# Performance work log

Measured on AMD Instinct MI355X. Metric: run time of the kernel, lower is better.

## Reference

```python
import jax, jax.numpy as jnp
import numpy as np

B_, L_, DM, DI, DS, DTR, DC = 1, 2048, 2048, 4096, 16, 128, 4


def setup_inputs() -> dict:
    key = jax.random.key(0)
    ks = jax.random.split(key, 8)
    s = lambda k, shape, scale: jax.random.normal(k, shape, jnp.float32) * scale
    inp = {
        "hidden_states": s(ks[0], (B_, L_, DM), 1.0),
        "in_proj_weight": s(ks[1], (2 * DI, DM), DM ** -0.5),
        "conv1d_weight": s(ks[2], (DI, 1, DC), DC ** -0.5),
        "x_proj_weight": s(ks[3], (DTR + 2 * DS, DI), DI ** -0.5),
        "dt_proj_weight": s(ks[4], (DI, DTR), DTR ** -0.5),
        "out_proj_weight": s(ks[5], (DM, DI), DI ** -0.5),
    }
    # dt_proj_bias = inverse-softplus of dt ~ LogUniform[1e-3, 0.1] (as in init_dtprojbias)
    dt = jnp.exp(jax.random.uniform(ks[6], (DI,), jnp.float32) * (np.log(0.1) - np.log(0.001)) + np.log(0.001))
    dt = jnp.clip(dt, 1e-4, None)
    inp["dt_proj_bias"] = dt + jnp.log(-jnp.expm1(-dt))
    # A_log init: log of repeat(arange(1, d_state+1)) per d_inner row
    inp["A_log"] = jnp.log(jnp.tile(jnp.arange(1, DS + 1, dtype=jnp.float32), (DI, 1)))
    inp["D"] = jnp.ones((DI,), jnp.float32)
    return inp


def reference(hidden_states, in_proj_weight, conv1d_weight, x_proj_weight,
              dt_proj_weight, dt_proj_bias, A_log, D, out_proj_weight):
    b, l, dm = hidden_states.shape
    di, ds = A_log.shape
    # in_proj: [b,l,dm] -> xz [b, 2*di, l]
    xz = jnp.einsum('ed,bld->bel', in_proj_weight, hidden_states)
    x, z = xz[:, :di], xz[:, di:]
    # depthwise causal conv1d (pad left d_conv-1, no bias) + SiLU
    x = jax.lax.conv_general_dilated(
        x, conv1d_weight, window_strides=(1,), padding=[(DC - 1, 0)],
        dimension_numbers=('NCH', 'OIH', 'NCH'), feature_group_count=di)
    x = jax.nn.silu(x)  # [b, di, l]
    # x_proj -> dt, B, C
    x_dbl = jnp.einsum('pd,bdl->blp', x_proj_weight, x)  # [b,l,dtr+2*ds]
    dt, Bc, Cc = jnp.split(x_dbl, [DTR, DTR + ds], axis=-1)
    delta = jnp.einsum('dr,blr->bld', dt_proj_weight, dt) + dt_proj_bias
    delta = jax.nn.softplus(delta)  # delta_softplus=True, delta_bias applied
    A = -jnp.exp(A_log)  # [di, ds]
    u = jnp.transpose(x, (0, 2, 1))  # [b,l,di]

    def step(h, inputs):
        d_t, B_t, C_t, u_t = inputs  # [b,di],[b,ds],[b,ds],[b,di]
        dA = jnp.exp(d_t[..., None] * A)                      # [b,di,ds]
        h = h * dA + (d_t * u_t)[..., None] * B_t[:, None, :]  # [b,di,ds]
        y = jnp.einsum('bdn,bn->bd', h, C_t)
        return h, y

    h0 = jnp.zeros((b, di, ds), hidden_states.dtype)
    xs = (jnp.swapaxes(delta, 0, 1), jnp.swapaxes(Bc, 0, 1),
          jnp.swapaxes(Cc, 0, 1), jnp.swapaxes(u, 0, 1))
    _, ys = jax.lax.scan(step, h0, xs)          # [l,b,di]
    y = jnp.swapaxes(ys, 0, 1) + u * D          # skip term u*D
    y = y * jax.nn.silu(jnp.transpose(z, (0, 2, 1)))  # gate
    return jnp.einsum('md,bld->blm', out_proj_weight, y)
```

## Files before the change

### kernel.cpp

```cpp
#include <hip/hip_runtime.h>
#include <hip/hip_bf16.h>

#define LSEQ 2048
#define DMODEL 2048
#define DINNER 4096
#define DSTATE 16
#define DTRANK 128
#define DCONV 4
#define DXP (DTRANK + 2*DSTATE)
#define NCHUNK 64
#define LCHUNK (LSEQ / NCHUNK)
#define KSPLIT 16

using bf16 = __hip_bfloat16;
typedef __attribute__((ext_vector_type(8))) short short8;
typedef __attribute__((ext_vector_type(4))) float float4v;

__device__ __forceinline__ float b2f(bf16 v) { return __bfloat162float(v); }
__device__ __forceinline__ bf16 f2b(float v) { return __float2bfloat16(v); }
__device__ __forceinline__ float bl16(unsigned u) { return __uint_as_float(u << 16); }
__device__ __forceinline__ float bh16(unsigned u) { return __uint_as_float(u & 0xffff0000u); }

__device__ __forceinline__ short f2bs(float v) {
    bf16 b = __float2bfloat16(v);
    union { bf16 b; short s; } u; u.b = b; return u.s;
}

__device__ __forceinline__ float fsilu(float x) {
    return x * __builtin_amdgcn_rcpf(1.0f + __expf(-x));
}

__device__ __forceinline__ short8 ld8(const float* p) {
    float4v f0 = *(const float4v*)p;
    float4v f1 = *(const float4v*)(p + 4);
    short8 r;
    r[0] = f2bs(f0[0]); r[1] = f2bs(f0[1]); r[2] = f2bs(f0[2]); r[3] = f2bs(f0[3]);
    r[4] = f2bs(f1[0]); r[5] = f2bs(f1[1]); r[6] = f2bs(f1[2]); r[7] = f2bs(f1[3]);
    return r;
}
__device__ __forceinline__ short8 ld8(const bf16* p) { return *(const short8*)p; }

template<typename CT> __device__ __forceinline__ CT cvtC(float v);
template<> __device__ __forceinline__ bf16  cvtC<bf16>(float v)  { return f2b(v); }
template<> __device__ __forceinline__ float cvtC<float>(float v) { return v; }

template<typename T> __device__ __forceinline__ float cvtL(T v);
template<> __device__ __forceinline__ float cvtL<bf16>(bf16 v)   { return b2f(v); }
template<> __device__ __forceinline__ float cvtL<float>(float v) { return v; }

__device__ __forceinline__ void glds16(const bf16* g, void* lds_base) {
    __builtin_amdgcn_global_load_lds(
        (const __attribute__((address_space(1))) void*)g,
        (__attribute__((address_space(3))) void*)lds_base, 16, 0, 0);
}

__global__ __launch_bounds__(256) void cvt4(
    const float* __restrict__ s0, bf16* __restrict__ d0, int n0,
    const float* __restrict__ s1, bf16* __restrict__ d1, int n1,
    const float* __restrict__ s2, bf16* __restrict__ d2, int n2,
    const float* __restrict__ s3, bf16* __restrict__ d3, int n3)
{
    const int b = blockIdx.x;
    const int nb0 = n0 >> 11, nb1 = n1 >> 11, nb2 = n2 >> 11;
    const float* s; bf16* d; int i;
    if (b < nb0)                  { s = s0; d = d0; i = b * 2048; }
    else if (b < nb0 + nb1)       { s = s1; d = d1; i = (b - nb0) * 2048; }
    else if (b < nb0 + nb1 + nb2) { s = s2; d = d2; i = (b - nb0 - nb1) * 2048; }
    else                          { s = s3; d = d3; i = (b - nb0 - nb1 - nb2) * 2048; }
    i += threadIdx.x * 8;
    *(short8*)(d + i) = ld8(s + i);
}

__global__ __launch_bounds__(256) void cvt1(
    const float* __restrict__ src, bf16* __restrict__ dst, int n)
{
    int i = (blockIdx.x * 256 + threadIdx.x) * 8;
    if (i >= n) return;
    *(short8*)(dst + i) = ld8(src + i);
}

#define GBAR  __builtin_amdgcn_s_barrier()
#define VMW4  asm volatile("s_waitcnt vmcnt(4)" ::: "memory")
#define VMW8  asm volatile("s_waitcnt vmcnt(8)" ::: "memory")
#define VMW0  asm volatile("s_waitcnt vmcnt(0)" ::: "memory")

#define LDA8(BASE, RB, AF) do {                                                \
  _Pragma("unroll") for (int mi_ = 0; mi_ < 4; ++mi_)                          \
  _Pragma("unroll") for (int kk_ = 0; kk_ < 2; ++kk_)                          \
    AF[mi_][kk_] = *(const short8*)((BASE) + (((RB) + mi_*16 + t16) << 6)      \
                                    + ((((kk_*4) + quad) ^ sw7) << 3));        \
} while (0)

#define LDB4(BASE, RB, BF) do {                                                \
  _Pragma("unroll") for (int nj_ = 0; nj_ < 2; ++nj_)                          \
  _Pragma("unroll") for (int kk_ = 0; kk_ < 2; ++kk_)                          \
    BF[nj_][kk_] = *(const short8*)((BASE) + (((RB) + nj_*16 + t16) << 6)      \
                                    + ((((kk_*4) + quad) ^ sw7) << 3));        \
} while (0)

#define MM16(AF, BF, MO, NO) do {                                              \
  _Pragma("unroll") for (int kk_ = 0; kk_ < 2; ++kk_)                          \
  _Pragma("unroll") for (int mi_ = 0; mi_ < 4; ++mi_)                          \
  _Pragma("unroll") for (int nj_ = 0; nj_ < 2; ++nj_)                          \
    acc[(MO)+mi_][(NO)+nj_] = __builtin_amdgcn_mfma_f32_16x16x32_bf16(         \
        AF[mi_][kk_], BF[nj_][kk_], acc[(MO)+mi_][(NO)+nj_], 0, 0, 0);         \
} while (0)

#define ST_ALO(tau) do { size_t ko_ = (size_t)(tau) << 6; int bo_ = ((tau)&1) << 15; \
  glds16(sA +       ko_, dA0 + bo_);                                           \
  glds16(sA + oA1 + ko_, dA1 + bo_); } while (0)
#define ST_AHI(tau) do { size_t ko_ = (size_t)(tau) << 6; int bo_ = ((tau)&1) << 15; \
  glds16(sA + oA2 + ko_, dA2 + bo_);                                           \
  glds16(sA + oA3 + ko_, dA3 + bo_); } while (0)
#define ST_BLO(tau) do { size_t ko_ = (size_t)(tau) << 6; int bo_ = ((tau)&1) << 15; \
  glds16(sB +       ko_, dB0 + bo_);                                           \
  glds16(sB + oB1 + ko_, dB1 + bo_); } while (0)
#define ST_BHI(tau) do { size_t ko_ = (size_t)(tau) << 6; int bo_ = ((tau)&1) << 15; \
  glds16(sB + oB2 + ko_, dB2 + bo_);                                           \
  glds16(sB + oB3 + ko_, dB3 + bo_); } while (0)

#define KSTEP(T, BI) do {                                                      \
    const bf16* Ab = As[BI];                                                   \
    const bf16* Bb = Bs[BI];                                                   \
    short8 af[4][2], b0[2][2], b1[2][2];                                       \
                                       \
    LDA8(Ab, wm, af);                                                          \
    LDB4(Bb, wn, b0);                                                          \
    if ((T) + 1 < NT) { ST_AHI((T) + 1); ST_BLO((T) + 1); }                    \
    __builtin_amdgcn_s_setprio(1); MM16(af, b0, 0, 0);                         \
    __builtin_amdgcn_s_setprio(0); GBAR;                                       \
                    \
    LDB4(Bb, wn + 32, b1);                                                     \
    if ((T) + 2 < NT) ST_ALO((T) + 2);                                         \
    __builtin_amdgcn_s_setprio(1); MM16(af, b1, 0, 2);                         \
    __builtin_amdgcn_s_setprio(0); GBAR;                                       \
                           \
    LDA8(Ab, wm + 64, af);                                                     \
    if ((T) + 2 < NT) ST_BHI((T) + 2);                                         \
    __builtin_amdgcn_s_setprio(1); MM16(af, b1, 4, 2);                         \
    __builtin_amdgcn_s_setprio(0); GBAR;                                       \
                                   \
    __builtin_amdgcn_s_setprio(1); MM16(af, b0, 4, 0);                         \
    __builtin_amdgcn_s_setprio(0);                                             \
    if ((T) + 2 < NT) { VMW4; } else { VMW0; }                                 \
    GBAR;                                                                      \
} while (0)

#define GEMM_PRO_COMMON                                                        \
    const int t    = threadIdx.x;                                              \
    const int wave = t >> 6;                                                   \
    const int lane = t & 63;                                                   \
    const int t16  = lane & 15;                                                \
    const int quad = lane >> 4;                                                \
    const int sw7  = t16 & 7;                                                  \
    const int wm   = (wave >> 2) * 128;                                        \
    const int wn   = (wave & 3) * 64;                                          \
    const int lrow  = lane >> 3;                                               \
    const int lseg  = lane & 7;                                                \
    const int segx  = (lseg ^ lrow) * 8;                                       \
    const int bwoff = (wave & 3) * 8 + (wave >> 2) * 64;

#define GEMM_LDS_DSTS                                                          \
    char* dA0 = (char*)&As[0][(  0 + wave * 8) * 64];                          \
    char* dA1 = (char*)&As[0][(128 + wave * 8) * 64];                          \
    char* dA2 = (char*)&As[0][( 64 + wave * 8) * 64];                          \
    char* dA3 = (char*)&As[0][(192 + wave * 8) * 64];                          \
    char* dB0 = (char*)&Bs[0][(  0 + bwoff) * 64];                             \
    char* dB1 = (char*)&Bs[0][(128 + bwoff) * 64];                             \
    char* dB2 = (char*)&Bs[0][( 32 + bwoff) * 64];                             \
    char* dB3 = (char*)&Bs[0][(160 + bwoff) * 64];

__global__ __launch_bounds__(512, 2) void gemm_inproj(
    const bf16* __restrict__ A, int lda,
    const bf16* __restrict__ B, int ldb,
    bf16* __restrict__ C, int ldc, int K)
{
    __shared__ __align__(16) bf16 As[2][256 * 64];
    __shared__ __align__(16) bf16 Bs[2][256 * 64];
    GEMM_PRO_COMMON
    const int bid = blockIdx.x;
    const int s   = (bid & 7) * (gridDim.x >> 3) + (bid >> 3);
    const int bm0 = (s & 7) << 8;
    const int bn0 = (s >> 3) << 8;

    const bf16* sA = A + (size_t)(bm0 + wave * 8 + lrow) * lda + segx;
    const bf16* sB = B + (size_t)(bn0 + bwoff + lrow) * ldb + segx;
    const size_t oA1 = (size_t)128 * lda, oA2 = (size_t)64 * lda, oA3 = (size_t)192 * lda;
    const size_t oB1 = (size_t)128 * ldb, oB2 = (size_t)32 * ldb, oB3 = (size_t)160 * ldb;
    GEMM_LDS_DSTS

    const int NT = K >> 6;

    float4v acc[8][4];
#pragma unroll
    for (int i = 0; i < 8; ++i)
#pragma unroll
        for (int j = 0; j < 4; ++j) acc[i][j] = (float4v)(0.0f);

    ST_ALO(0); ST_AHI(0); ST_BLO(0); ST_BHI(0);
    if (NT > 1) { ST_ALO(1); ST_BHI(1); VMW4; } else { VMW0; }
    GBAR;

    for (int T = 0; T < NT; T += 2) {
        KSTEP(T, 0);
        KSTEP(T + 1, 1);
    }

#pragma unroll
    for (int mi = 0; mi < 8; ++mi) {
#pragma unroll
        for (int nj = 0; nj < 4; ++nj) {
            const int m_base = bm0 + wm + (mi >> 2) * 64 + (mi & 3) * 16 + quad * 4;
            const int n_g    = bn0 + wn + (nj >> 1) * 32 + (nj & 1) * 16 + t16;
#pragma unroll
            for (int r = 0; r < 4; ++r)
                C[(size_t)(m_base + r) * ldc + n_g] = f2b(acc[mi][nj][r]);
        }
    }
}

#define OST(tau, BI) do { size_t ko_ = (size_t)(tau) << 6;                     \
  _Pragma("unroll") for (int g_ = 0; g_ < 4; ++g_) {                           \
    glds16(Ag[g_] + ko_, Ad[g_] + (BI) * 16384);                               \
    glds16(Bg[g_] + ko_, Bd[g_] + (BI) * 16384); } } while (0)

#define OKSTEP(T, BI) do {                                                     \
    const bf16* Ab = &As[BI][0];                                               \
    const bf16* Bb = &Bs[BI][0];                                               \
    short8 a_[4][2], b_[4][2];                                                 \
    _Pragma("unroll") for (int mi_ = 0; mi_ < 4; ++mi_)                        \
    _Pragma("unroll") for (int kk_ = 0; kk_ < 2; ++kk_)                        \
      a_[mi_][kk_] = *(const short8*)(Ab + ((wm + mi_*16 + t16) << 6)          \
                                      + ((((kk_*4) + quad) ^ sw) << 3));       \
    _Pragma("unroll") for (int nj_ = 0; nj_ < 4; ++nj_)                        \
    _Pragma("unroll") for (int kk_ = 0; kk_ < 2; ++kk_)                        \
      b_[nj_][kk_] = *(const short8*)(Bb + ((wn + nj_*16 + t16) << 6)          \
                                      + ((((kk_*4) + quad) ^ sw) << 3));       \
    if ((T) + 2 < NT) OST((T) + 2, ((BI) + 2) % 3);                            \
    __builtin_amdgcn_s_setprio(1);                                             \
    _Pragma("unroll") for (int kk_ = 0; kk_ < 2; ++kk_)                        \
    _Pragma("unroll") for (int mi_ = 0; mi_ < 4; ++mi_)                        \
    _Pragma("unroll") for (int nj_ = 0; nj_ < 4; ++nj_)                        \
      acc[mi_][nj_] = __builtin_amdgcn_mfma_f32_16x16x32_bf16(                 \
          a_[mi_][kk_], b_[nj_][kk_], acc[mi_][nj_], 0, 0, 0);                 \
    __builtin_amdgcn_s_setprio(0);                                             \
    if ((T) + 2 < NT) { VMW8; }                                                \
    else if ((T) + 1 < NT) { VMW0; }                                           \
    GBAR;                                                                      \
} while (0)

__global__ __launch_bounds__(256, 1) void gemm_outproj(
    const bf16* __restrict__ A, int lda,
    const bf16* __restrict__ B, int ldb,
    float* __restrict__ C, int ldc, int K)
{
    __shared__ __align__(16) bf16 As[3][128 * 64];
    __shared__ __align__(16) bf16 Bs[3][128 * 64];

    const int t    = threadIdx.x;
    const int wave = t >> 6;
    const int lane = t & 63;
    const int t16  = lane & 15;
    const int quad = lane >> 4;
    const int sw   = t16 & 7;
    const int wm   = (wave >> 1) * 64;
    const int wn   = (wave & 1) * 64;

    const int bid = blockIdx.x;
    const int m_t = ((bid & 1) << 3) | ((bid >> 3) & 7);
    const int n_t = (((bid >> 1) & 3) << 2) | ((bid >> 6) & 3);
    const int bm0 = m_t << 7;
    const int bn0 = n_t << 7;

    const int lrow = lane >> 3;
    const int gseg = ((lane & 7) ^ lrow) * 8;

    const bf16* Ag[4]; char* Ad[4];
#pragma unroll
    for (int g = 0; g < 4; g++) {
        int r = wave * 32 + g * 8;
        Ag[g] = A + (size_t)(bm0 + r + lrow) * lda + gseg;
        Ad[g] = (char*)&As[0][0] + r * 128;
    }
    const bf16* Bg[4]; char* Bd[4];
#pragma unroll
    for (int g = 0; g < 4; g++) {
        int r = wave * 32 + g * 8;
        Bg[g] = B + (size_t)(bn0 + r + lrow) * ldb + gseg;
        Bd[g] = (char*)&Bs[0][0] + r * 128;
    }

    const int NT = K >> 6;

    float4v acc[4][4];
#pragma unroll
    for (int i = 0; i < 4; i++)
#pragma unroll
        for (int j = 0; j < 4; j++) acc[i][j] = (float4v)(0.0f);

    OST(0, 0);
    OST(1, 1);
    VMW8;
    GBAR;

    for (int T = 0; T + 2 < NT; T += 3) {
        OKSTEP(T, 0);
        OKSTEP(T + 1, 1);
        OKSTEP(T + 2, 2);
    }
    OKSTEP(NT - 1, 0);

#pragma unroll
    for (int mi = 0; mi < 4; mi++) {
#pragma unroll
        for (int nj = 0; nj < 4; nj++) {
            int n_g = bn0 + wn + nj * 16 + t16;
#pragma unroll
            for (int r = 0; r < 4; r++) {
                int m_g = bm0 + wm + mi * 16 + quad * 4 + r;
                C[(size_t)m_g * ldc + n_g] = acc[mi][nj][r];
            }
        }
    }
}

__global__ __launch_bounds__(256) void gemm_xproj(
    const bf16* __restrict__ A, int lda,
    const bf16* __restrict__ B, int ldb,
    float* __restrict__ P)
{
    __shared__ bf16 As[128][64];
    __shared__ bf16 Bs[160][64];

    const int t    = threadIdx.x;
    const int wave = t >> 6;
    const int lane = t & 63;
    const int t16  = lane & 15;
    const int quad = lane >> 4;
    const int wm   = (wave >> 1) * 64;
    const int wn   = (wave & 1) * 80;
    const int bm0  = blockIdx.x * 128;
    const int kbeg = blockIdx.y * (DINNER / KSPLIT);

    const int lrow = lane >> 3;
    const int gseg = ((lane & 7) ^ lrow) * 8;

    const bf16* Ag[4]; char* Ad[4];
#pragma unroll
    for (int g = 0; g < 4; g++) {
        int r = wave * 32 + g * 8;
        Ag[g] = A + (size_t)(bm0 + r + lrow) * lda + gseg + kbeg;
        Ad[g] = (char*)As + r * 128;
    }
    const bf16* Bg[5]; char* Bd[5];
#pragma unroll
    for (int g = 0; g < 5; g++) {
        int r = wave * 40 + g * 8;
        Bg[g] = B + (size_t)(r + lrow) * ldb + gseg + kbeg;
        Bd[g] = (char*)Bs + r * 128;
    }

    float4v acc[4][5];
#pragma unroll
    for (int i = 0; i < 4; i++)
#pragma unroll
        for (int j = 0; j < 5; j++) acc[i][j] = (float4v)(0.0f);

    const int sw = t16 & 7;

    for (int k0 = 0; k0 < DINNER / KSPLIT; k0 += 64) {
        __syncthreads();
#pragma unroll
        for (int g = 0; g < 4; g++) glds16(Ag[g] + k0, Ad[g]);
#pragma unroll
        for (int g = 0; g < 5; g++) glds16(Bg[g] + k0, Bd[g]);
        __syncthreads();

#pragma unroll
        for (int kk = 0; kk < 2; kk++) {
            const int kso = ((kk * 4 + quad) ^ sw) * 8;
            short8 a[4], b[5];
#pragma unroll
            for (int mi = 0; mi < 4; mi++)
                a[mi] = *(const short8*)(&As[wm + mi * 16 + t16][kso]);
#pragma unroll
            for (int nj = 0; nj < 5; nj++)
                b[nj] = *(const short8*)(&Bs[wn + nj * 16 + t16][kso]);
#pragma unroll
            for (int mi = 0; mi < 4; mi++)
#pragma unroll
                for (int nj = 0; nj < 5; nj++)
                    acc[mi][nj] = __builtin_amdgcn_mfma_f32_16x16x32_bf16(
                        a[mi], b[nj], acc[mi][nj], 0, 0, 0);
        }
    }

    float* Pk = P + (size_t)blockIdx.y * LSEQ * DXP;
#pragma unroll
    for (int mi = 0; mi < 4; mi++) {
#pragma unroll
        for (int nj = 0; nj < 5; nj++) {
            int n_g = wn + nj * 16 + t16;
#pragma unroll
            for (int r = 0; r < 4; r++) {
                int m_g = bm0 + wm + mi * 16 + quad * 4 + r;
                Pk[(size_t)m_g * DXP + n_g] = acc[mi][nj][r];
            }
        }
    }
}

template<int BN, typename CT, bool SP>
__global__ __launch_bounds__(256) void gemm_glds64(
    const bf16* __restrict__ A, int lda,
    const bf16* __restrict__ B, int ldb,
    CT* __restrict__ C, int ldc,
    int K, const float* __restrict__ bias)
{
    constexpr int NJ  = BN / 32;
    constexpr int BGL = BN / 32;
    __shared__ bf16 As[128][64];
    __shared__ bf16 Bs[BN][64];

    const int t    = threadIdx.x;
    const int wave = t >> 6;
    const int lane = t & 63;
    const int t16  = lane & 15;
    const int quad = lane >> 4;
    const int wm   = (wave >> 1) * 64;
    const int wn   = (wave & 1) * (BN / 2);
    const int bm0  = blockIdx.x * 128;
    const int bn0  = blockIdx.y * BN;

    const int lrow = lane >> 3;
    const int gseg = (((lane & 7) ^ lrow) * 8);

    const bf16* Ag[4]; char* Ad[4];
#pragma unroll
    for (int g = 0; g < 4; g++) {
        Ag[g] = A + (size_t)(bm0 + wave * 32 + g * 8 + lrow) * lda + gseg;
        Ad[g] = (char*)As + (wave * 32 + g * 8) * 128;
    }
    const bf16* Bg[BGL]; char* Bd[BGL];
#pragma unroll
    for (int g = 0; g < BGL; g++) {
        int r = (BN == 128) ? (wave * 32 + g * 8) : (wave * 16 + g * 8);
        Bg[g] = B + (size_t)(bn0 + r + lrow) * ldb + gseg;
        Bd[g] = (char*)Bs + r * 128;
    }

    float4v acc[4][NJ];
#pragma unroll
    for (int i = 0; i < 4; i++)
#pragma unroll
        for (int j = 0; j < NJ; j++) acc[i][j] = (float4v)(0.0f);

    const int sw = t16 & 7;

    for (int k0 = 0; k0 < K; k0 += 64) {
        __syncthreads();
#pragma unroll
        for (int g = 0; g < 4; g++)   glds16(Ag[g] + k0, Ad[g]);
#pragma unroll
        for (int g = 0; g < BGL; g++) glds16(Bg[g] + k0, Bd[g]);
        __syncthreads();

#pragma unroll
        for (int kk = 0; kk < 2; kk++) {
            const int kso = ((kk * 4 + quad) ^ sw) * 8;
            short8 a[4], b[NJ];
#pragma unroll
            for (int mi = 0; mi < 4; mi++)
                a[mi] = *(const short8*)(&As[wm + mi * 16 + t16][kso]);
#pragma unroll
            for (int nj = 0; nj < NJ; nj++)
                b[nj] = *(const short8*)(&Bs[wn + nj * 16 + t16][kso]);
#pragma unroll
            for (int mi = 0; mi < 4; mi++)
#pragma unroll
                for (int nj = 0; nj < NJ; nj++)
                    acc[mi][nj] = __builtin_amdgcn_mfma_f32_16x16x32_bf16(
                        a[mi], b[nj], acc[mi][nj], 0, 0, 0);
        }
    }

#pragma unroll
    for (int mi = 0; mi < 4; mi++) {
#pragma unroll
        for (int nj = 0; nj < NJ; nj++) {
            int n_g = bn0 + wn + nj * 16 + t16;
            float bia = SP ? bias[n_g] : 0.0f;
#pragma unroll
            for (int r = 0; r < 4; r++) {
                int m_g = bm0 + wm + mi * 16 + quad * 4 + r;
                float v = acc[mi][nj][r];
                if (SP) {
                    float x = v + bia;
                    v = (x > 20.0f) ? x : __logf(1.0f + __expf(x));
                }
                C[(size_t)m_g * ldc + n_g] = cvtC<CT>(v);
            }
        }
    }
}

template<typename AT, typename CT, bool SP>
__global__ __launch_bounds__(256) void gemm_bt(
    const AT* __restrict__ A, int lda,
    const float* __restrict__ B, int ldb,
    CT* __restrict__ C, int ldc,
    int M, int N, int K,
    const float* __restrict__ bias)
{
    __shared__ bf16 As[64][40];
    __shared__ bf16 Bs[64][40];

    const int t    = threadIdx.x;
    const int bm0  = blockIdx.x * 64;
    const int bn0  = blockIdx.y * 64;
    const int row  = t >> 2;
    const int seg  = (t & 3) * 8;
    const int wave = t >> 6;
    const int lane = t & 63;
    const int wm   = (wave >> 1) * 32;
    const int wn   = (wave & 1) * 32;
    const int t16  = lane & 15;
    const int quad = lane >> 4;

    float4v acc[2][2];
#pragma unroll
    for (int i = 0; i < 2; i++)
#pragma unroll
        for (int j = 0; j < 2; j++) acc[i][j] = (float4v)(0.0f);

    const AT*    Aptr = A + (size_t)(bm0 + row) * lda + seg;
    const float* Bptr = B + (size_t)(bn0 + row) * ldb + seg;
    const bool a_ok = (bm0 + row) < M;
    const bool b_ok = (bn0 + row) < N;
    const short8 zero8 = (short8)(0);

    for (int k0 = 0; k0 < K; k0 += 32) {
        short8 av = a_ok ? ld8(Aptr + k0) : zero8;
        short8 bv = b_ok ? ld8(Bptr + k0) : zero8;
        __syncthreads();
        *(short8*)(&As[row][seg]) = av;
        *(short8*)(&Bs[row][seg]) = bv;
        __syncthreads();

        short8 a0 = *(const short8*)(&As[wm + t16][quad * 8]);
        short8 a1 = *(const short8*)(&As[wm + 16 + t16][quad * 8]);
        short8 b0 = *(const short8*)(&Bs[wn + t16][quad * 8]);
        short8 b1 = *(const short8*)(&Bs[wn + 16 + t16][quad * 8]);
        acc[0][0] = __builtin_amdgcn_mfma_f32_16x16x32_bf16(a0, b0, acc[0][0], 0, 0, 0);
        acc[0][1] = __builtin_amdgcn_mfma_f32_16x16x32_bf16(a0, b1, acc[0][1], 0, 0, 0);
        acc[1][0] = __builtin_amdgcn_mfma_f32_16x16x32_bf16(a1, b0, acc[1][0], 0, 0, 0);
        acc[1][1] = __builtin_amdgcn_mfma_f32_16x16x32_bf16(a1, b1, acc[1][1], 0, 0, 0);
    }

#pragma unroll
    for (int i = 0; i < 2; i++) {
#pragma unroll
        for (int j = 0; j < 2; j++) {
            int n_g = bn0 + wn + j * 16 + t16;
            if (n_g >= N) continue;
            float bia = SP ? bias[n_g] : 0.0f;
#pragma unroll
            for (int r = 0; r < 4; r++) {
                int m_g = bm0 + wm + i * 16 + quad * 4 + r;
                if (m_g >= M) continue;
                float v = acc[i][j][r];
                if (SP) {
                    float x = v + bia;
                    v = (x > 20.0f) ? x : log1pf(__expf(x));
                }
                C[(size_t)m_g * ldc + n_g] = cvtC<CT>(v);
            }
        }
    }
}

__global__ __launch_bounds__(256) void reduce_splitk(
    const float* __restrict__ P, bf16* __restrict__ C, float* __restrict__ bc, int MN)
{
    int i = blockIdx.x * 256 + threadIdx.x;
    if (i >= MN) return;
    float s = 0.f;
#pragma unroll
    for (int ks = 0; ks < KSPLIT; ks++) s += P[(size_t)ks * MN + i];
    C[i] = f2b(s);
    int l = i / DXP;
    int p = i - l * DXP;
    if (p >= DTRANK) bc[l * 32 + (p - DTRANK)] = s;
}

__global__ __launch_bounds__(256) void conv_silu_par(
    const bf16* __restrict__ xz, const float* __restrict__ w, bf16* __restrict__ xc)
{
    const int d  = blockIdx.x * 256 + threadIdx.x;
    const int lc = blockIdx.y * 64;
    const float w0 = w[d * 4 + 0];
    const float w1 = w[d * 4 + 1];
    const float w2 = w[d * 4 + 2];
    const float w3 = w[d * 4 + 3];
    const size_t S = 2 * DINNER;
    const bf16* p = xz + d;
    float xm3 = 0.f, xm2 = 0.f, xm1 = 0.f;
    if (lc >= 3) {
        xm3 = b2f(p[(size_t)(lc - 3) * S]);
        xm2 = b2f(p[(size_t)(lc - 2) * S]);
        xm1 = b2f(p[(size_t)(lc - 1) * S]);
    }
    for (int l = lc; l < lc + 64; ++l) {
        float x0 = b2f(p[(size_t)l * S]);
        float a = w0 * xm3 + w1 * xm2 + w2 * xm1 + w3 * x0;
        xc[(size_t)l * DINNER + d] = f2b(fsilu(a));
        xm3 = xm2; xm2 = xm1; xm1 = x0;
    }
}

__global__ __launch_bounds__(256) void conv_silu_inplace(
    bf16* __restrict__ xz, const float* __restrict__ w)
{
    const int d = blockIdx.x * 256 + threadIdx.x;
    const float w0 = w[d * 4 + 0];
    const float w1 = w[d * 4 + 1];
    const float w2 = w[d * 4 + 2];
    const float w3 = w[d * 4 + 3];
    bf16* p = xz + d;
    const size_t S = 2 * DINNER;
    float xm3 = 0.f, xm2 = 0.f, xm1 = 0.f;
    for (int l = 0; l < LSEQ; l += 4) {
        float x0 = b2f(p[(size_t)(l + 0) * S]);
        float x1 = b2f(p[(size_t)(l + 1) * S]);
        float x2 = b2f(p[(size_t)(l + 2) * S]);
        float x3 = b2f(p[(size_t)(l + 3) * S]);
        float a0 = w0 * xm3 + w1 * xm2 + w2 * xm1 + w3 * x0;
        float a1 = w0 * xm2 + w1 * xm1 + w2 * x0  + w3 * x1;
        float a2 = w0 * xm1 + w1 * x0  + w2 * x1  + w3 * x2;
        float a3 = w0 * x0  + w1 * x1  + w2 * x2  + w3 * x3;
        p[(size_t)(l + 0) * S] = f2b(a0 / (1.0f + __expf(-a0)));
        p[(size_t)(l + 1) * S] = f2b(a1 / (1.0f + __expf(-a1)));
        p[(size_t)(l + 2) * S] = f2b(a2 / (1.0f + __expf(-a2)));
        p[(size_t)(l + 3) * S] = f2b(a3 / (1.0f + __expf(-a3)));
        xm3 = x1; xm2 = x2; xm1 = x3;
    }
}

__global__ __launch_bounds__(256) void scan_chunk1(
    const float* __restrict__ dlt, const bf16* __restrict__ xc,
    const float* __restrict__ bc, const float* __restrict__ A_log,
    float* __restrict__ hend, float* __restrict__ Pbuf)
{
    const int d = blockIdx.x * 256 + threadIdx.x;
    const int c = blockIdx.y;

    float Ac[16];
    {
        const float* ap = A_log + d * DSTATE;
#pragma unroll
        for (int i = 0; i < 16; i++) Ac[i] = -__expf(ap[i]);
    }

    float h[16];
#pragma unroll
    for (int i = 0; i < 16; i++) h[i] = 0.f;
    float sdelta = 0.f;

    const float* pd = dlt + (size_t)c * LCHUNK * DINNER + d;
    const bf16*  pu = xc  + (size_t)c * LCHUNK * DINNER + d;
    const float* pb = bc  + (size_t)c * LCHUNK * 32;

#pragma unroll 2
    for (int l = 0; l < LCHUNK; ++l) {
        const float delta = *pd;
        const float u     = b2f(*pu);
        const float du    = delta * u;
        sdelta += delta;
        float4v B0 = *(const float4v*)pb;
        float4v B1 = *(const float4v*)(pb + 4);
        float4v B2 = *(const float4v*)(pb + 8);
        float4v B3 = *(const float4v*)(pb + 12);
#pragma unroll
        for (int i = 0; i < 16; i++) {
            float dA = __expf(delta * Ac[i]);
            float Bi = (i < 4) ? B0[i] : (i < 8) ? B1[i - 4] : (i < 12) ? B2[i - 8] : B3[i - 12];
            h[i] = h[i] * dA + du * Bi;
        }
        pd += DINNER; pu += DINNER; pb += 32;
    }

    float* hp = hend + ((size_t)c * DINNER + d) * DSTATE;
    float* pp = Pbuf + ((size_t)c * DINNER + d) * DSTATE;
#pragma unroll
    for (int q = 0; q < 4; q++) {
        float4v hv, pv;
#pragma unroll
        for (int j = 0; j < 4; j++) {
            hv[j] = h[q * 4 + j];
            pv[j] = __expf(sdelta * Ac[q * 4 + j]);
        }
        *(float4v*)(hp + q * 4) = hv;
        *(float4v*)(pp + q * 4) = pv;
    }
}

__global__ __launch_bounds__(256) void scan_combine(
    float* __restrict__ hend, const float* __restrict__ Pbuf)
{
    const int dn = blockIdx.x * 256 + threadIdx.x;
    const size_t STR = (size_t)DINNER * DSTATE;
    float H = 0.f;
    size_t idx = dn;
    for (int c0 = 0; c0 < NCHUNK; c0 += 8) {
        float he[8], pp[8];
#pragma unroll
        for (int j = 0; j < 8; j++) {
            he[j] = hend[idx + (size_t)j * STR];
            pp[j] = Pbuf[idx + (size_t)j * STR];
        }
#pragma unroll
        for (int j = 0; j < 8; j++) {
            hend[idx + (size_t)j * STR] = H;
            H = he[j] + pp[j] * H;
        }
        idx += 8 * STR;
    }
}

__global__ __launch_bounds__(256) void scan_chunk2(
    const float* __restrict__ dlt, const bf16* __restrict__ xc,
    bf16* __restrict__ xz, const float* __restrict__ bc,
    const float* __restrict__ A_log, const float* __restrict__ Dp,
    const float* __restrict__ Hin)
{
    const int d = blockIdx.x * 256 + threadIdx.x;
    const int c = blockIdx.y;

    float Ac[16];
    {
        const float* ap = A_log + d * DSTATE;
#pragma unroll
        for (int i = 0; i < 16; i++) Ac[i] = -__expf(ap[i]);
    }
    const float Dv = Dp[d];

    float h[16];
    {
        const float* hp = Hin + ((size_t)c * DINNER + d) * DSTATE;
#pragma unroll
        for (int q = 0; q < 4; q++) {
            float4v hv = *(const float4v*)(hp + q * 4);
#pragma unroll
            for (int j = 0; j < 4; j++) h[q * 4 + j] = hv[j];
        }
    }

    const float* pd = dlt + (size_t)c * LCHUNK * DINNER + d;
    const bf16*  pu = xc  + (size_t)c * LCHUNK * DINNER + d;
    const float* pb = bc  + (size_t)c * LCHUNK * 32;
    bf16*        pz = xz  + (size_t)c * LCHUNK * (2 * DINNER) + DINNER + d;

#pragma unroll 2
    for (int l = 0; l < LCHUNK; ++l) {
        const float delta = *pd;
        const float u     = b2f(*pu);
        const float du    = delta * u;
        float4v B0 = *(const float4v*)pb;
        float4v B1 = *(const float4v*)(pb + 4);
        float4v B2 = *(const float4v*)(pb + 8);
        float4v B3 = *(const float4v*)(pb + 12);
        float4v C0 = *(const float4v*)(pb + 16);
        float4v C1 = *(const float4v*)(pb + 20);
        float4v C2 = *(const float4v*)(pb + 24);
        float4v C3 = *(const float4v*)(pb + 28);
        float yv = 0.f;
#pragma unroll
        for (int i = 0; i < 16; i++) {
            float dA = __expf(delta * Ac[i]);
            float Bi = (i < 4) ? B0[i] : (i < 8) ? B1[i - 4] : (i < 12) ? B2[i - 8] : B3[i - 12];
            float Ci = (i < 4) ? C0[i] : (i < 8) ? C1[i - 4] : (i < 12) ? C2[i - 8] : C3[i - 12];
            h[i] = h[i] * dA + du * Bi;
            yv += h[i] * Ci;
        }
        yv += u * Dv;
        float z = b2f(*pz);
        yv *= fsilu(z);
        *pz = f2b(yv);
        pd += DINNER; pu += DINNER; pb += 32; pz += 2 * DINNER;
    }
}

template<typename DT>
__global__ __launch_bounds__(256) void scan_serial(
    const DT* __restrict__ dlt, bf16* __restrict__ xz,
    const bf16* __restrict__ xdbl,
    const float* __restrict__ A_log, const float* __restrict__ Dp)
{
    const int nq = threadIdx.x & 3;
    const int d  = blockIdx.x * 64 + (threadIdx.x >> 2);
    float Ac[4];
#pragma unroll
    for (int i = 0; i < 4; i++)
        Ac[i] = -__expf(A_log[d * DSTATE + nq * 4 + i]);
    const float Dv = Dp[d];
    float h[4] = {0.f, 0.f, 0.f, 0.f};
    for (int l = 0; l < LSEQ; ++l) {
        const float delta = cvtL<DT>(dlt[(size_t)l * DINNER + d]);
        const float u     = b2f(xz[(size_t)l * (2 * DINNER) + d]);
        const uint2 qb = *(const uint2*)(xdbl + (size_t)l * DXP + DTRANK + nq * 4);
        const uint2 qc = *(const uint2*)(xdbl + (size_t)l * DXP + DTRANK + DSTATE + nq * 4);
        float Bv[4] = { bl16(qb.x), bh16(qb.x), bl16(qb.y), bh16(qb.y) };
        float Cv[4] = { bl16(qc.x), bh16(qc.x), bl16(qc.y), bh16(qc.y) };
        const float du = delta * u;
        float yv = 0.f;
#pragma unroll
        for (int i = 0; i < 4; i++) {
            float dA = __expf(delta * Ac[i]);
            h[i] = h[i] * dA + du * Bv[i];
            yv += h[i] * Cv[i];
        }
        yv += __shfl_xor(yv, 1);
        yv += __shfl_xor(yv, 2);
        if (nq == 0) {
            yv += u * Dv;
            bf16* zp = xz + (size_t)l * (2 * DINNER) + DINNER + d;
            float z = b2f(*zp);
            yv *= z / (1.0f + __expf(-z));
            *zp = f2b(yv);
        }
    }
}

extern "C" void kernel_launch(void* const* d_in, const int* in_sizes, int n_in,
                              void* d_out, int out_size, void* d_ws, size_t ws_size,
                              hipStream_t stream)
{
    const float* hs      = (const float*)d_in[0];
    const float* w_in    = (const float*)d_in[1];
    const float* w_conv  = (const float*)d_in[2];
    const float* w_xproj = (const float*)d_in[3];
    const float* w_dt    = (const float*)d_in[4];
    const float *w_out, *b_dt, *A_log, *Dp;
    if (in_sizes[5] == DMODEL * DINNER) {
        w_out = (const float*)d_in[5];
        b_dt  = (const float*)d_in[6];
        A_log = (const float*)d_in[7];
        Dp    = (const float*)d_in[8];
    } else {
        b_dt  = (const float*)d_in[5];
        A_log = (const float*)d_in[6];
        Dp    = (const float*)d_in[7];
        w_out = (const float*)d_in[8];
    }
    float* out = (float*)d_out;

    const size_t SZ_XZ   = (size_t)LSEQ * 2 * DINNER * sizeof(bf16);
    const size_t SZ_XC   = (size_t)LSEQ * DINNER * sizeof(bf16);
    const size_t SZ_XDBL = (size_t)LSEQ * DXP * sizeof(bf16);
    const size_t SZ_DLTF = (size_t)LSEQ * DINNER * sizeof(float);
    const size_t SZ_HP   = (size_t)NCHUNK * DINNER * DSTATE * sizeof(float);
    const size_t SZ_BC   = (size_t)LSEQ * 32 * sizeof(float);

    char* p = (char*)d_ws;
    bf16* xz = (bf16*)p; p += SZ_XZ;

    const size_t need_fast = SZ_XZ + SZ_XC + SZ_XDBL + SZ_DLTF + 2 * SZ_HP + SZ_BC;
    const bool fast = ws_size >= need_fast;

    dim3 blk(256);

    if (fast) {
        bf16*  xc   = (bf16*)p;  p += SZ_XC;
        bf16*  xdbl = (bf16*)p;  p += SZ_XDBL;
        char*  hpr  = p;         p += SZ_DLTF;
        char*  dreg = p;
        float* dlt  = (float*)hpr;
        float* hend = (float*)dreg;
        float* Pbuf = (float*)(dreg + SZ_HP);
        float* bcb  = (float*)(dreg + 2 * SZ_HP);

        bf16*  w_in_b  = (bf16*)hpr;
        float* xp_part = (float*)hpr;
        bf16*  hs_b    = (bf16*)dreg;
        bf16*  w_dt_b  = (bf16*)(dreg + (size_t)LSEQ * DMODEL * sizeof(bf16));
        bf16*  w_xp_b  = (bf16*)(dreg + (size_t)LSEQ * DMODEL * sizeof(bf16)
                                      + (size_t)DINNER * DTRANK * sizeof(bf16));
        bf16*  w_out_b = (bf16*)xc;

        {
            int n0 = 2 * DINNER * DMODEL, n1 = LSEQ * DMODEL;
            int n2 = DINNER * DTRANK,     n3 = DXP * DINNER;
            cvt4<<<dim3((n0 + n1 + n2 + n3) / 2048), blk, 0, stream>>>(
                w_in, w_in_b, n0, hs, hs_b, n1, w_dt, w_dt_b, n2, w_xproj, w_xp_b, n3);
        }

        gemm_inproj<<<dim3(256), dim3(512), 0, stream>>>(
            hs_b, DMODEL, w_in_b, DMODEL, xz, 2*DINNER, DMODEL);

        conv_silu_par<<<dim3(DINNER/256, LSEQ/64), blk, 0, stream>>>(xz, w_conv, xc);

        gemm_xproj<<<dim3(LSEQ/128, KSPLIT), blk, 0, stream>>>(
            xc, DINNER, w_xp_b, DINNER, xp_part);
        reduce_splitk<<<dim3((LSEQ * DXP + 255) / 256), blk, 0, stream>>>(
            xp_part, xdbl, bcb, LSEQ * DXP);

        gemm_glds64<128, float, true><<<dim3(LSEQ/128, DINNER/128), blk, 0, stream>>>(
            xdbl, DXP, w_dt_b, DTRANK, dlt, DINNER, DTRANK, b_dt);

        scan_chunk1<<<dim3(DINNER/256, NCHUNK), blk, 0, stream>>>(
            dlt, xc, bcb, A_log, hend, Pbuf);
        scan_combine<<<dim3(DINNER*DSTATE/256), blk, 0, stream>>>(hend, Pbuf);
        scan_chunk2<<<dim3(DINNER/256, NCHUNK), blk, 0, stream>>>(
            dlt, xc, xz, bcb, A_log, Dp, hend);

        cvt1<<<dim3((DMODEL*DINNER)/2048), blk, 0, stream>>>(w_out, w_out_b, DMODEL*DINNER);
        gemm_outproj<<<dim3(256), blk, 0, stream>>>(
            xz + DINNER, 2*DINNER, w_out_b, DINNER, out, DMODEL, DINNER);
    } else {
        bf16* xdbl = (bf16*)p; p += SZ_XDBL;
        size_t used = (size_t)(p - (char*)d_ws);
        bool dlt_f32 = (ws_size - used) >= SZ_DLTF;

        gemm_bt<float, bf16, false><<<dim3(LSEQ/64, (2*DINNER)/64), blk, 0, stream>>>(
            hs, DMODEL, w_in, DMODEL, xz, 2*DINNER, LSEQ, 2*DINNER, DMODEL, nullptr);
        conv_silu_inplace<<<dim3(DINNER/256), blk, 0, stream>>>(xz, w_conv);
        gemm_bt<bf16, bf16, false><<<dim3(LSEQ/64, 3), blk, 0, stream>>>(
            xz, 2*DINNER, w_xproj, DINNER, xdbl, DXP, LSEQ, DXP, DINNER, nullptr);
        if (dlt_f32) {
            float* dlt = (float*)p;
            gemm_bt<bf16, float, true><<<dim3(LSEQ/64, DINNER/64), blk, 0, stream>>>(
                xdbl, DXP, w_dt, DTRANK, dlt, DINNER, LSEQ, DINNER, DTRANK, b_dt);
            scan_serial<float><<<dim3(DINNER/64), blk, 0, stream>>>(dlt, xz, xdbl, A_log, Dp);
        } else {
            bf16* dlt = (bf16*)p;
            gemm_bt<bf16, bf16, true><<<dim3(LSEQ/64, DINNER/64), blk, 0, stream>>>(
                xdbl, DXP, w_dt, DTRANK, dlt, DINNER, LSEQ, DINNER, DTRANK, b_dt);
            scan_serial<bf16><<<dim3(DINNER/64), blk, 0, stream>>>(dlt, xz, xdbl, A_log, Dp);
        }
        gemm_bt<bf16, float, false><<<dim3(LSEQ/64, DMODEL/64), blk, 0, stream>>>(
            xz + DINNER, 2*DINNER, w_out, DINNER, out, DMODEL, LSEQ, DMODEL, DINNER, nullptr);
    }
}
```

Baseline: 392.6 us.

## Restructure GEMM k-step pipeline, specialize dt_proj GEMM, halve scan chunks

The main GEMM k-step now issues both B fragment loads up front and prefetches all of the next tile's A-high and B stages together, which cuts the barrier phases from four to two and lowers the vmcnt wait threshold. The dt_proj GEMM becomes a dedicated kernel that loads the full K=128 slice of A and B into LDS once, then runs all MFMAs without a k-loop or repeated syncs. The scan chunk count drops from 64 to 32, giving fewer chunk-combine states in exchange for longer serial chunks and fewer blocks. These changes target barrier overhead and launch parallelism, but they change how loads overlap with compute, which may expose load latency.

```diff
diff --git a/kernel.cpp b/kernel.cpp
--- a/kernel.cpp
+++ b/kernel.cpp
@@ -8,7 +8,7 @@
 #define DTRANK 128
 #define DCONV 4
 #define DXP (DTRANK + 2*DSTATE)
-#define NCHUNK 64
+#define NCHUNK 32
 #define LCHUNK (LSEQ / NCHUNK)
 #define KSPLIT 16
 
@@ -80,7 +80,7 @@
 }
 
 #define GBAR  __builtin_amdgcn_s_barrier()
-#define VMW4  asm volatile("s_waitcnt vmcnt(4)" ::: "memory")
+#define VMW2  asm volatile("s_waitcnt vmcnt(2)" ::: "memory")
 #define VMW8  asm volatile("s_waitcnt vmcnt(8)" ::: "memory")
 #define VMW0  asm volatile("s_waitcnt vmcnt(0)" ::: "memory")
 
@@ -123,26 +123,21 @@
     const bf16* Ab = As[BI];                                                   \
     const bf16* Bb = Bs[BI];                                                   \
     short8 af[4][2], b0[2][2], b1[2][2];                                       \
-                                       \
+                \
     LDA8(Ab, wm, af);                                                          \
     LDB4(Bb, wn, b0);                                                          \
-    if ((T) + 1 < NT) { ST_AHI((T) + 1); ST_BLO((T) + 1); }                    \
-    __builtin_amdgcn_s_setprio(1); MM16(af, b0, 0, 0);                         \
+    LDB4(Bb, wn + 32, b1);                                                     \
+    if ((T) + 1 < NT) { ST_AHI((T) + 1); ST_BLO((T) + 1); ST_BHI((T) + 1); }   \
+    __builtin_amdgcn_s_setprio(1);                                             \
+    MM16(af, b0, 0, 0); MM16(af, b1, 0, 2);                                    \
     __builtin_amdgcn_s_setprio(0); GBAR;                                       \
-                    \
-    LDB4(Bb, wn + 32, b1);                                                     \
+                        \
+    LDA8(Ab, wm + 64, af);                                                     \
     if ((T) + 2 < NT) ST_ALO((T) + 2);                                         \
-    __builtin_amdgcn_s_setprio(1); MM16(af, b1, 0, 2);                         \
-    __builtin_amdgcn_s_setprio(0); GBAR;                                       \
-                           \
-    LDA8(Ab, wm + 64, af);                                                     \
-    if ((T) + 2 < NT) ST_BHI((T) + 2);                                         \
-    __builtin_amdgcn_s_setprio(1); MM16(af, b1, 4, 2);                         \
-    __builtin_amdgcn_s_setprio(0); GBAR;                                       \
-                                   \
-    __builtin_amdgcn_s_setprio(1); MM16(af, b0, 4, 0);                         \
+    __builtin_amdgcn_s_setprio(1);                                             \
+    MM16(af, b1, 4, 2); MM16(af, b0, 4, 0);                                    \
     __builtin_amdgcn_s_setprio(0);                                             \
-    if ((T) + 2 < NT) { VMW4; } else { VMW0; }                                 \
+    if ((T) + 2 < NT) { VMW2; } else { VMW0; }                                 \
     GBAR;                                                                      \
 } while (0)
 
@@ -198,7 +193,7 @@
         for (int j = 0; j < 4; ++j) acc[i][j] = (float4v)(0.0f);
 
     ST_ALO(0); ST_AHI(0); ST_BLO(0); ST_BHI(0);
-    if (NT > 1) { ST_ALO(1); ST_BHI(1); VMW4; } else { VMW0; }
+    if (NT > 1) { ST_ALO(1); VMW2; } else { VMW0; }
     GBAR;
 
     for (int T = 0; T < NT; T += 2) {
@@ -410,17 +405,14 @@
     }
 }
 
-template<int BN, typename CT, bool SP>
-__global__ __launch_bounds__(256) void gemm_glds64(
-    const bf16* __restrict__ A, int lda,
-    const bf16* __restrict__ B, int ldb,
-    CT* __restrict__ C, int ldc,
-    int K, const float* __restrict__ bias)
-{
-    constexpr int NJ  = BN / 32;
-    constexpr int BGL = BN / 32;
-    __shared__ bf16 As[128][64];
-    __shared__ bf16 Bs[BN][64];
+__global__ __launch_bounds__(256) void gemm_dtproj(
+    const bf16* __restrict__ A,
+    const bf16* __restrict__ B,
+    float* __restrict__ C,
+    const float* __restrict__ bias)
+{
+    __shared__ __align__(16) bf16 As[128][128];
+    __shared__ __align__(16) bf16 Bs[128][128];
 
     const int t    = threadIdx.x;
     const int wave = t >> 6;
@@ -428,77 +420,59 @@
     const int t16  = lane & 15;
     const int quad = lane >> 4;
     const int wm   = (wave >> 1) * 64;
-    const int wn   = (wave & 1) * (BN / 2);
+    const int wn   = (wave & 1) * 64;
     const int bm0  = blockIdx.x * 128;
-    const int bn0  = blockIdx.y * BN;
-
-    const int lrow = lane >> 3;
-    const int gseg = (((lane & 7) ^ lrow) * 8);
-
-    const bf16* Ag[4]; char* Ad[4];
-#pragma unroll
-    for (int g = 0; g < 4; g++) {
-        Ag[g] = A + (size_t)(bm0 + wave * 32 + g * 8 + lrow) * lda + gseg;
-        Ad[g] = (char*)As + (wave * 32 + g * 8) * 128;
-    }
-    const bf16* Bg[BGL]; char* Bd[BGL];
-#pragma unroll
-    for (int g = 0; g < BGL; g++) {
-        int r = (BN == 128) ? (wave * 32 + g * 8) : (wave * 16 + g * 8);
-        Bg[g] = B + (size_t)(bn0 + r + lrow) * ldb + gseg;
-        Bd[g] = (char*)Bs + r * 128;
-    }
-
-    float4v acc[4][NJ];
+    const int bn0  = blockIdx.y * 128;
+
+    const int srow = wave * 4 + (lane >> 4);
+    const int scol = ((lane & 15) ^ srow) * 8;
+
+#pragma unroll
+    for (int g = 0; g < 8; g++) {
+        glds16(A + (size_t)(bm0 + g * 16 + srow) * DXP + scol,
+               (char*)As + (g * 16 + wave * 4) * 256);
+        glds16(B + (size_t)(bn0 + g * 16 + srow) * DTRANK + scol,
+               (char*)Bs + (g * 16 + wave * 4) * 256);
+    }
+    VMW0;
+    GBAR;
+
+    float4v acc[4][4];
 #pragma unroll
     for (int i = 0; i < 4; i++)
 #pragma unroll
-        for (int j = 0; j < NJ; j++) acc[i][j] = (float4v)(0.0f);
-
-    const int sw = t16 & 7;
-
-    for (int k0 = 0; k0 < K; k0 += 64) {
-        __syncthreads();
-#pragma unroll
-        for (int g = 0; g < 4; g++)   glds16(Ag[g] + k0, Ad[g]);
-#pragma unroll
-        for (int g = 0; g < BGL; g++) glds16(Bg[g] + k0, Bd[g]);
-        __syncthreads();
-
-#pragma unroll
-        for (int kk = 0; kk < 2; kk++) {
-            const int kso = ((kk * 4 + quad) ^ sw) * 8;
-            short8 a[4], b[NJ];
-#pragma unroll
-            for (int mi = 0; mi < 4; mi++)
-                a[mi] = *(const short8*)(&As[wm + mi * 16 + t16][kso]);
-#pragma unroll
-            for (int nj = 0; nj < NJ; nj++)
-                b[nj] = *(const short8*)(&Bs[wn + nj * 16 + t16][kso]);
-#pragma unroll
-            for (int mi = 0; mi < 4; mi++)
-#pragma unroll
-                for (int nj = 0; nj < NJ; nj++)
-                    acc[mi][nj] = __builtin_amdgcn_mfma_f32_16x16x32_bf16(
-                        a[mi], b[nj], acc[mi][nj], 0, 0, 0);
-        }
+        for (int j = 0; j < 4; j++) acc[i][j] = (float4v)(0.0f);
+
+#pragma unroll
+    for (int kk = 0; kk < 4; kk++) {
+        const int kso = ((kk * 4 + quad) ^ t16) * 8;
+        short8 a[4], b[4];
+#pragma unroll
+        for (int mi = 0; mi < 4; mi++)
+            a[mi] = *(const short8*)(&As[wm + mi * 16 + t16][kso]);
+#pragma unroll
+        for (int nj = 0; nj < 4; nj++)
+            b[nj] = *(const short8*)(&Bs[wn + nj * 16 + t16][kso]);
+#pragma unroll
+        for (int mi = 0; mi < 4; mi++)
+#pragma unroll
+            for (int nj = 0; nj < 4; nj++)
+                acc[mi][nj] = __builtin_amdgcn_mfma_f32_16x16x32_bf16(
+                    a[mi], b[nj], acc[mi][nj], 0, 0, 0);
     }
 
 #pragma unroll
     for (int mi = 0; mi < 4; mi++) {
 #pragma unroll
-        for (int nj = 0; nj < NJ; nj++) {
+        for (int nj = 0; nj < 4; nj++) {
             int n_g = bn0 + wn + nj * 16 + t16;
-            float bia = SP ? bias[n_g] : 0.0f;
+            float bia = bias[n_g];
 #pragma unroll
             for (int r = 0; r < 4; r++) {
                 int m_g = bm0 + wm + mi * 16 + quad * 4 + r;
-                float v = acc[mi][nj][r];
-                if (SP) {
-                    float x = v + bia;
-                    v = (x > 20.0f) ? x : __logf(1.0f + __expf(x));
-                }
-                C[(size_t)m_g * ldc + n_g] = cvtC<CT>(v);
+                float x = acc[mi][nj][r] + bia;
+                float v = (x > 20.0f) ? x : __logf(1.0f + __expf(x));
+                C[(size_t)m_g * DINNER + n_g] = v;
             }
         }
     }
@@ -904,8 +878,8 @@
         reduce_splitk<<<dim3((LSEQ * DXP + 255) / 256), blk, 0, stream>>>(
             xp_part, xdbl, bcb, LSEQ * DXP);
 
-        gemm_glds64<128, float, true><<<dim3(LSEQ/128, DINNER/128), blk, 0, stream>>>(
-            xdbl, DXP, w_dt_b, DTRANK, dlt, DINNER, DTRANK, b_dt);
+        gemm_dtproj<<<dim3(LSEQ/128, DINNER/128), blk, 0, stream>>>(
+            xdbl, w_dt_b, dlt, b_dt);
 
         scan_chunk1<<<dim3(DINNER/256, NCHUNK), blk, 0, stream>>>(
             dlt, xc, bcb, A_log, hend, Pbuf);
```

Result: slower. 405.4 us (+3.3%).
